# Kernel optimization log

Hardware: AMD Instinct MI355X
Metric: run time of the kernel (lower is better)

Reference implementation:

```python
import jax, jax.numpy as jnp
import numpy as np

D, OUT, IN = 64, 2048, 2048  # directions, out_features, in_features


def setup_inputs() -> dict:
    key = jax.random.key(0)
    k1, k2, k3 = jax.random.split(key, 3)
    # weight_noise: Bernoulli(sigmoid(weight)) bit samples, one (OUT, IN) binary matrix per direction.
    # Represented as 0/1 float32 (the CUDA kernel stores them bit-packed in int64 words).
    weight_noise = jax.random.bernoulli(k1, 0.5, (D, OUT, IN)).astype(jnp.float32)
    # Boolean input vector per direction (the kernel packs this to int64 words too).
    x = jax.random.bernoulli(k2, 0.5, (D, IN))
    # bias_noise = bias + (U[0,1) - 0.5) * noise_scale, with bias initialized to in_features/2.
    noise_scale = 1.0
    bias_noise = (IN / 2.0 + (jax.random.uniform(k3, (D, OUT)) - 0.5) * noise_scale).astype(jnp.float32)
    return {"weight_noise": weight_noise, "x": x, "bias_noise": bias_noise}


def reference(weight_noise, x, bias_noise):
    # binary_bmm: per-direction popcount matvec -> activation[d, o] = sum_i (W[d,o,i] & x[d,i]).
    # With 0/1 floats this is exactly a batched matvec.
    act = jnp.einsum('doi,di->do', weight_noise, x.astype(jnp.float32))  # [D, OUT]
    # threshold=True branch: boolean output (activation > bias_noise)
    return act > bias_noise
```

## Files before the change

### kernel.cpp

```cpp
#include <hip/hip_runtime.h>


#define NDIR 64
#define NOUT 2048
#define NIN  2048

typedef float f4 __attribute__((ext_vector_type(4)));

__global__ __launch_bounds__(256) void binlin_kernel(
    const float* __restrict__ W,
    const unsigned char* __restrict__ X,
    const float* __restrict__ B,
    float* __restrict__ out)
{
    const int lane = threadIdx.x & 63;
    const int wave = threadIdx.x >> 6;
    const int row  = blockIdx.x * 4 + wave;
    const int d    = row >> 11;

    const unsigned int probe = ((const unsigned int*)X)[lane];
    const bool x_is_float = (__ballot(probe == 0x3F800000u) != 0ull);
    const bool x_is_bytes = !x_is_float && (__ballot(probe > 1u) != 0ull);

    const f4* w4 = (const f4*)(W + (size_t)row * NIN);

    f4 w[8];
    #pragma unroll
    for (int j = 0; j < 8; ++j)
        w[j] = __builtin_nontemporal_load(&w4[j * 64 + lane]);

    unsigned int g[8];
    if (x_is_float) {
        const f4* xf = (const f4*)X + (size_t)d * (NIN / 4);
        #pragma unroll
        for (int j = 0; j < 8; ++j) {
            const f4 xv = xf[j * 64 + lane];
            g[j] = (unsigned)(xv.x != 0.0f)        | ((unsigned)(xv.y != 0.0f) << 1)
                 | ((unsigned)(xv.z != 0.0f) << 2) | ((unsigned)(xv.w != 0.0f) << 3);
        }
    } else if (x_is_bytes) {
        const unsigned int* x4 = (const unsigned int*)(X + (size_t)d * NIN);
        #pragma unroll
        for (int j = 0; j < 8; ++j) {
            const unsigned int xb = x4[j * 64 + lane];
            g[j] = ((xb & 0x000000ffu) ? 1u : 0u) | ((xb & 0x0000ff00u) ? 2u : 0u)
                 | ((xb & 0x00ff0000u) ? 4u : 0u) | ((xb & 0xff000000u) ? 8u : 0u);
        }
    } else {
        const int* xi = (const int*)X + (size_t)d * NIN;
        #pragma unroll
        for (int j = 0; j < 8; ++j) {
            const int i4 = (j * 64 + lane) * 4;
            g[j] = (xi[i4+0] ? 1u : 0u) | (xi[i4+1] ? 2u : 0u)
                 | (xi[i4+2] ? 4u : 0u) | (xi[i4+3] ? 8u : 0u);
        }
    }

    float acc = 0.0f;
    #pragma unroll
    for (int j = 0; j < 8; ++j) {
        acc += (g[j] & 1u) ? w[j].x : 0.0f;
        acc += (g[j] & 2u) ? w[j].y : 0.0f;
        acc += (g[j] & 4u) ? w[j].z : 0.0f;
        acc += (g[j] & 8u) ? w[j].w : 0.0f;
    }

    #pragma unroll
    for (int off = 32; off > 0; off >>= 1)
        acc += __shfl_down(acc, off, 64);

    if (lane == 0)
        out[row] = (acc > B[row]) ? 1.0f : 0.0f;
}

extern "C" void kernel_launch(void* const* d_in, const int* in_sizes, int n_in,
                              void* d_out, int out_size, void* d_ws, size_t ws_size,
                              hipStream_t stream) {
    const float*         W = (const float*)d_in[0];
    const unsigned char* X = (const unsigned char*)d_in[1];
    const float*         B = (const float*)d_in[2];
    float*               O = (float*)d_out;

    const int rows = NDIR * NOUT;
    binlin_kernel<<<dim3(rows / 4), dim3(256), 0, stream>>>(W, X, B, O);
}
```

Baseline: 1.265 ms.

## Process sixteen rows per wave with double-buffered weight prefetch

Each wave now handles sixteen consecutive rows instead of one, decoding the input bit vector once and reusing it across rows. Weight rows are loaded into two register buffers alternately so the next row's loads are in flight while the current row is reduced. This targets per-wave setup overhead and poor memory-level parallelism in a bandwidth-bound matvec, at the cost of more registers and fewer blocks.

```diff
diff --git a/kernel.cpp b/kernel.cpp
--- a/kernel.cpp
+++ b/kernel.cpp
@@ -4,8 +4,35 @@
 #define NDIR 64
 #define NOUT 2048
 #define NIN  2048
+#define ROWS_PER_WAVE 16
+#define NBLOCKS ((NDIR * NOUT) / ROWS_PER_WAVE / 4)
 
 typedef float f4 __attribute__((ext_vector_type(4)));
+
+#define LOADW(buf, r) do {                                                  \
+    const f4* p_ = wbase + (size_t)(r) * (NIN / 4);                         \
+    _Pragma("unroll")                                                       \
+    for (int j = 0; j < 8; ++j)                                             \
+        buf[j] = __builtin_nontemporal_load(&p_[j * 64 + lane]);            \
+  } while (0)
+
+#define COMPUTE(buf, r) do {                                                \
+    float acc_ = 0.0f;                                                      \
+    _Pragma("unroll")                                                       \
+    for (int j = 0; j < 8; ++j) {                                           \
+        acc_ += (g[j] & 1u) ? buf[j].x : 0.0f;                              \
+        acc_ += (g[j] & 2u) ? buf[j].y : 0.0f;                              \
+        acc_ += (g[j] & 4u) ? buf[j].z : 0.0f;                              \
+        acc_ += (g[j] & 8u) ? buf[j].w : 0.0f;                              \
+    }                                                                       \
+    _Pragma("unroll")                                                       \
+    for (int off_ = 32; off_ > 0; off_ >>= 1)                               \
+        acc_ += __shfl_down(acc_, off_, 64);                                \
+    if (lane == 0) {                                                        \
+        const int rr_ = row0 + (r);                                         \
+        out[rr_] = (acc_ > B[rr_]) ? 1.0f : 0.0f;                           \
+    }                                                                       \
+  } while (0)
 
 __global__ __launch_bounds__(256) void binlin_kernel(
     const float* __restrict__ W,
@@ -15,19 +42,13 @@
 {
     const int lane = threadIdx.x & 63;
     const int wave = threadIdx.x >> 6;
-    const int row  = blockIdx.x * 4 + wave;
-    const int d    = row >> 11;
+    const int wgid = blockIdx.x * 4 + wave;
+    const int row0 = wgid * ROWS_PER_WAVE;
+    const int d    = row0 >> 11;
 
     const unsigned int probe = ((const unsigned int*)X)[lane];
     const bool x_is_float = (__ballot(probe == 0x3F800000u) != 0ull);
     const bool x_is_bytes = !x_is_float && (__ballot(probe > 1u) != 0ull);
-
-    const f4* w4 = (const f4*)(W + (size_t)row * NIN);
-
-    f4 w[8];
-    #pragma unroll
-    for (int j = 0; j < 8; ++j)
-        w[j] = __builtin_nontemporal_load(&w4[j * 64 + lane]);
 
     unsigned int g[8];
     if (x_is_float) {
@@ -56,21 +77,18 @@
         }
     }
 
-    float acc = 0.0f;
+    const f4* wbase = (const f4*)(W + (size_t)row0 * NIN);
+
+    f4 wA[8], wB[8];
+    LOADW(wA, 0);
+    LOADW(wB, 1);
     #pragma unroll
-    for (int j = 0; j < 8; ++j) {
-        acc += (g[j] & 1u) ? w[j].x : 0.0f;
-        acc += (g[j] & 2u) ? w[j].y : 0.0f;
-        acc += (g[j] & 4u) ? w[j].z : 0.0f;
-        acc += (g[j] & 8u) ? w[j].w : 0.0f;
+    for (int k = 0; k < ROWS_PER_WAVE - 2; k += 2) {
+        COMPUTE(wA, k);     LOADW(wA, k + 2);
+        COMPUTE(wB, k + 1); LOADW(wB, k + 3);
     }
-
-    #pragma unroll
-    for (int off = 32; off > 0; off >>= 1)
-        acc += __shfl_down(acc, off, 64);
-
-    if (lane == 0)
-        out[row] = (acc > B[row]) ? 1.0f : 0.0f;
+    COMPUTE(wA, ROWS_PER_WAVE - 2);
+    COMPUTE(wB, ROWS_PER_WAVE - 1);
 }
 
 extern "C" void kernel_launch(void* const* d_in, const int* in_sizes, int n_in,
@@ -81,6 +99,5 @@
     const float*         B = (const float*)d_in[2];
     float*               O = (float*)d_out;
 
-    const int rows = NDIR * NOUT;
-    binlin_kernel<<<dim3(rows / 4), dim3(256), 0, stream>>>(W, X, B, O);
+    binlin_kernel<<<dim3(NBLOCKS), dim3(256), 0, stream>>>(W, X, B, O);
 }
```

Result: no change. 1.284 ms (+1.5%).
